# Kernel optimization log

Measured on AMD Instinct MI355X. Metric: run time of the kernel, lower is better.

Reference implementation:

```python
import jax, jax.numpy as jnp
import numpy as np

N_NODES = 50000
N_EDGES = 800000
IN_DIM = 58
HID = 100


def _agnn_prop(x, src, dst, beta, num_nodes):
    """PyG AGNNConv: cosine-similarity attention, softmax over in-edges, scatter-add."""
    # F.normalize(x, p=2, dim=-1) with eps clamp
    norm = jnp.sqrt(jnp.sum(x * x, axis=-1, keepdims=True))
    xn = x / jnp.maximum(norm, 1e-12)
    # per-edge attention logit: beta * cos(x_i, x_j)  (i=dst, j=src)
    alpha = beta * jnp.sum(xn[src] * xn[dst], axis=-1)  # [E]
    # numerically stable softmax grouped by destination node
    m = jax.ops.segment_max(alpha, dst, num_segments=num_nodes)  # [N]
    e = jnp.exp(alpha - m[dst])
    den = jax.ops.segment_sum(e, dst, num_segments=num_nodes)  # [N]
    w = e / (den[dst] + 1e-16)  # [E]
    # attention-weighted aggregation of source features
    return jax.ops.segment_sum(x[src] * w[:, None], dst, num_segments=num_nodes)


def setup_inputs() -> dict:
    key = jax.random.key(0)
    ks = jax.random.split(key, 6)
    x = jax.random.normal(ks[0], (N_NODES, IN_DIM), dtype=jnp.float32)
    edge_index = jax.random.randint(ks[1], (2, N_EDGES), 0, N_NODES, dtype=jnp.int64)
    lin1_w = jax.random.normal(ks[2], (HID, IN_DIM), dtype=jnp.float32) * (1.0 / np.sqrt(IN_DIM))
    lin1_b = jax.random.normal(ks[3], (HID,), dtype=jnp.float32) * 0.01
    beta2 = jnp.ones((1,), dtype=jnp.float32)
    lin2_w = jax.random.normal(ks[4], (1, HID), dtype=jnp.float32) * (1.0 / np.sqrt(HID))
    lin2_b = jax.random.normal(ks[5], (1,), dtype=jnp.float32) * 0.01
    return {"x": x, "edge_index": edge_index, "lin1_w": lin1_w, "lin1_b": lin1_b,
            "beta2": beta2, "lin2_w": lin2_w, "lin2_b": lin2_b}


def reference(x, edge_index, lin1_w, lin1_b, beta2, lin2_w, lin2_b):
    num_nodes = x.shape[0]
    # eval mode: dropout is identity
    h = jax.nn.relu(x @ lin1_w.T + lin1_b)  # [N, 100]
    # AGNNConv adds self-loops by default
    loops = jnp.arange(num_nodes, dtype=edge_index.dtype)
    src = jnp.concatenate([edge_index[0], loops])
    dst = jnp.concatenate([edge_index[1], loops])
    h = _agnn_prop(h, src, dst, jnp.float32(1.0), num_nodes)  # prop1: beta fixed at 1
    h = _agnn_prop(h, src, dst, beta2[0], num_nodes)          # prop2: learnable beta
    return h @ lin2_w.T + lin2_b  # [N, 1]
```

## Files before the change

### kernel.cpp

```cpp
#include <hip/hip_runtime.h>
#include <hip/hip_fp16.h>

#define N_NODES 50000
#define E_BASE  800000
#define IN_DIM  58
#define HID     100
#define HP2     128
#define SCAN_BLOCKS ((N_NODES + 255) / 256)

__global__ __launch_bounds__(256) void lin1_kernel(
    const float* __restrict__ x, const float* __restrict__ w,
    const float* __restrict__ b, __half* __restrict__ h,
    float* __restrict__ invn) {
  __shared__ alignas(16) float xs[64 * IN_DIM];
  __shared__ alignas(16) float wsm[IN_DIM * HP2];
  __shared__ float bl[HP2];
  int tid = threadIdx.x;
  int nb = blockIdx.x * 64;
  for (int i = tid; i < 64 * IN_DIM; i += 256) {
    int g = nb * IN_DIM + i;
    xs[i] = (g < N_NODES * IN_DIM) ? x[g] : 0.f;
  }
  for (int i = tid; i < IN_DIM * HP2; i += 256) {
    int k = i / HP2, j = i - k * HP2;
    wsm[i] = (j < HID) ? w[j * IN_DIM + k] : 0.f;
  }
  if (tid < HP2) bl[tid] = (tid < HID) ? b[tid] : 0.f;
  __syncthreads();
  int t_j = tid & 15, t_n = tid >> 4;
  float acc[4][8];
#pragma unroll
  for (int ni = 0; ni < 4; ++ni)
#pragma unroll
    for (int j = 0; j < 8; ++j) acc[ni][j] = bl[8 * t_j + j];
  for (int k = 0; k < IN_DIM; ++k) {
    float xv[4];
#pragma unroll
    for (int ni = 0; ni < 4; ++ni) xv[ni] = xs[(4 * t_n + ni) * IN_DIM + k];
    float4 wa = *(const float4*)&wsm[k * HP2 + 8 * t_j];
    float4 wb = *(const float4*)&wsm[k * HP2 + 8 * t_j + 4];
    float wv[8] = {wa.x, wa.y, wa.z, wa.w, wb.x, wb.y, wb.z, wb.w};
#pragma unroll
    for (int ni = 0; ni < 4; ++ni)
#pragma unroll
      for (int j = 0; j < 8; ++j) acc[ni][j] = fmaf(xv[ni], wv[j], acc[ni][j]);
  }
#pragma unroll
  for (int ni = 0; ni < 4; ++ni) {
    int n = nb + 4 * t_n + ni;
    uint4 st;
    ushort* sp = (ushort*)&st;
    float ss = 0.f;
#pragma unroll
    for (int j = 0; j < 8; ++j) {
      float v = fmaxf(acc[ni][j], 0.f);
      __half hv = __float2half_rn(v);
      sp[j] = __half_as_ushort(hv);
      float vq = __half2float(hv);
      ss = fmaf(vq, vq, ss);
    }
#pragma unroll
    for (int off = 1; off < 16; off <<= 1) ss += __shfl_xor(ss, off);
    if (n < N_NODES) {
      *((uint4*)(h + (size_t)n * HP2) + t_j) = st;
      if (t_j == 0) invn[n] = 1.f / fmaxf(sqrtf(ss), 1e-12f);
    }
  }
}

__global__ __launch_bounds__(256) void hist_kernel(
    const int* __restrict__ ei, int* __restrict__ deg) {
  int i = blockIdx.x * 256 + threadIdx.x;
  if (i >= E_BASE / 4) return;
  int4 d4 = ((const int4*)(ei + E_BASE))[i];
  atomicAdd(&deg[d4.x], 1);
  atomicAdd(&deg[d4.y], 1);
  atomicAdd(&deg[d4.z], 1);
  atomicAdd(&deg[d4.w], 1);
}

__global__ __launch_bounds__(256) void scan_blocks_kernel(
    const int* __restrict__ deg, int* __restrict__ blocksum) {
  __shared__ int sh[4];
  int idx = blockIdx.x * 256 + threadIdx.x;
  int v = (idx < N_NODES) ? deg[idx] + 1 : 0;
#pragma unroll
  for (int off = 32; off; off >>= 1) v += __shfl_xor(v, off);
  if ((threadIdx.x & 63) == 0) sh[threadIdx.x >> 6] = v;
  __syncthreads();
  if (threadIdx.x == 0) blocksum[blockIdx.x] = sh[0] + sh[1] + sh[2] + sh[3];
}

__global__ __launch_bounds__(256) void scan_top_kernel(int* __restrict__ blocksum) {
  __shared__ int sh[256];
  int t = threadIdx.x;
  sh[t] = (t < SCAN_BLOCKS) ? blocksum[t] : 0;
  __syncthreads();
  for (int off = 1; off < 256; off <<= 1) {
    int v = (t >= off) ? sh[t - off] : 0;
    __syncthreads();
    sh[t] += v;
    __syncthreads();
  }
  if (t < SCAN_BLOCKS) blocksum[t] = (t == 0) ? 0 : sh[t - 1];
}

__global__ __launch_bounds__(256) void scan_apply_kernel(
    const int* __restrict__ deg, const int* __restrict__ blockoff,
    int* __restrict__ rowstart, int* __restrict__ cur,
    int* __restrict__ src_csr) {
  __shared__ int sh[256];
  int t = threadIdx.x;
  int idx = blockIdx.x * 256 + t;
  int v = (idx < N_NODES) ? deg[idx] + 1 : 0;
  sh[t] = v;
  __syncthreads();
  for (int off = 1; off < 256; off <<= 1) {
    int u = (t >= off) ? sh[t - off] : 0;
    __syncthreads();
    sh[t] += u;
    __syncthreads();
  }
  int excl = blockoff[blockIdx.x] + sh[t] - v;
  if (idx < N_NODES) {
    rowstart[idx] = excl;
    src_csr[excl] = idx;
    cur[idx] = excl + 1;
  }
  if (idx == N_NODES - 1) rowstart[N_NODES] = excl + v;
}

__global__ __launch_bounds__(256) void scatter_kernel(
    const int* __restrict__ ei, int* __restrict__ cur,
    int* __restrict__ src_csr) {
  int i = blockIdx.x * 256 + threadIdx.x;
  if (i >= E_BASE / 4) return;
  int4 s4 = ((const int4*)ei)[i];
  int4 d4 = ((const int4*)(ei + E_BASE))[i];
  int p;
  p = atomicAdd(&cur[d4.x], 1); src_csr[p] = s4.x;
  p = atomicAdd(&cur[d4.y], 1); src_csr[p] = s4.y;
  p = atomicAdd(&cur[d4.z], 1); src_csr[p] = s4.z;
  p = atomicAdd(&cur[d4.w], 1); src_csr[p] = s4.w;
}

template<bool WRITE_INVN, bool FINAL>
__global__ __launch_bounds__(256) void prop_kernel(
    const __half* __restrict__ h, const float* __restrict__ invn,
    const int* __restrict__ src_csr, const int* __restrict__ rowstart,
    const float* __restrict__ beta_ptr,
    __half* __restrict__ out_feat, float* __restrict__ out_invn,
    const float* __restrict__ w2, const float* __restrict__ b2,
    float* __restrict__ out_scalar) {
  int node = (blockIdx.x * 256 + threadIdx.x) >> 6;
  int lane = threadIdx.x & 63;
  if (node >= N_NODES) return;
  int lq = lane & 15, q = lane >> 4;
  float beta = beta_ptr ? beta_ptr[0] : 1.0f;
  float B = fabsf(beta);
  int start = rowstart[node], end = rowstart[node + 1];
  int deg = end - start;
  float ind = invn[node];
  uint4 dv = *((const uint4*)(h + (size_t)node * HP2) + lq);
  const __half* dh = (const __half*)&dv;
  float d[8];
#pragma unroll
  for (int j = 0; j < 8; ++j) d[j] = __half2float(dh[j]) * ind;
  float s = 0.f;
  float acc[8];
#pragma unroll
  for (int j = 0; j < 8; ++j) acc[j] = 0.f;
  int nt = (deg + 3) >> 2;
  for (int r = 0; r < nt; ++r) {
    int e = 4 * r + q;
    bool valid = e < deg;
    int p = start + (valid ? e : 0);
    int sn = src_csr[p];
    float iv = invn[sn];
    uint4 vv = *((const uint4*)(h + (size_t)sn * HP2) + lq);
    const __half* vh = (const __half*)&vv;
    float vf[8];
#pragma unroll
    for (int j = 0; j < 8; ++j) vf[j] = __half2float(vh[j]);
    float t = 0.f;
#pragma unroll
    for (int j = 0; j < 8; ++j) t = fmaf(vf[j], d[j], t);
#pragma unroll
    for (int off = 8; off; off >>= 1) t += __shfl_xor(t, off);
    float a = valid ? beta * t * iv : -1e30f;
    float wgt = __expf(a - B);
    s += wgt;
#pragma unroll
    for (int j = 0; j < 8; ++j) acc[j] = fmaf(wgt, vf[j], acc[j]);
  }
#pragma unroll
  for (int off = 16; off <= 32; off <<= 1) {
    s += __shfl_xor(s, off);
#pragma unroll
    for (int j = 0; j < 8; ++j) acc[j] += __shfl_xor(acc[j], off);
  }
  float invden = 1.f / (s + 1e-16f);
  if (!FINAL) {
    uint4 st;
    ushort* sp = (ushort*)&st;
    float ss = 0.f;
#pragma unroll
    for (int j = 0; j < 8; ++j) {
      __half hv = __float2half_rn(acc[j] * invden);
      sp[j] = __half_as_ushort(hv);
      float vq = __half2float(hv);
      ss = fmaf(vq, vq, ss);
    }
    if (q == 0) *((uint4*)(out_feat + (size_t)node * HP2) + lq) = st;
    if (WRITE_INVN) {
#pragma unroll
      for (int off = 1; off < 16; off <<= 1) ss += __shfl_xor(ss, off);
      if (lane == 0) out_invn[node] = 1.f / fmaxf(sqrtf(ss), 1e-12f);
    }
  } else {
    float qq = 0.f;
#pragma unroll
    for (int j = 0; j < 8; ++j) {
      int f = 8 * lq + j;
      float wv = (f < HID) ? w2[f] : 0.f;
      qq = fmaf(acc[j] * invden, wv, qq);
    }
#pragma unroll
    for (int off = 8; off; off >>= 1) qq += __shfl_xor(qq, off);
    if (lane == 0) out_scalar[node] = qq + b2[0];
  }
}

extern "C" void kernel_launch(void* const* d_in, const int* in_sizes, int n_in,
                              void* d_out, int out_size, void* d_ws, size_t ws_size,
                              hipStream_t stream) {
  const float* x      = (const float*)d_in[0];
  const int*   ei     = (const int*)d_in[1];
  const float* lin1_w = (const float*)d_in[2];
  const float* lin1_b = (const float*)d_in[3];
  const float* beta2  = (const float*)d_in[4];
  const float* lin2_w = (const float*)d_in[5];
  const float* lin2_b = (const float*)d_in[6];
  float* out = (float*)d_out;

  char* wsb = (char*)d_ws;
  __half* h1 = (__half*)wsb;                       wsb += (size_t)N_NODES * HP2 * 2;
  __half* h2 = (__half*)wsb;                       wsb += (size_t)N_NODES * HP2 * 2;
  float* invn1 = (float*)wsb;                      wsb += N_NODES * 4;
  float* invn2 = (float*)wsb;                      wsb += N_NODES * 4;
  int* deg      = (int*)wsb;                       wsb += N_NODES * 4;
  int* rowstart = (int*)wsb;                       wsb += (N_NODES + 1) * 4;
  int* cur      = (int*)wsb;                       wsb += N_NODES * 4;
  int* src_csr  = (int*)wsb;                       wsb += (size_t)(E_BASE + N_NODES) * 4;
  int* blocksum = (int*)wsb;                       wsb += SCAN_BLOCKS * 4;

  lin1_kernel<<<(N_NODES + 63) / 64, 256, 0, stream>>>(x, lin1_w, lin1_b, h1, invn1);

  hipMemsetAsync(deg, 0, N_NODES * sizeof(int), stream);
  hist_kernel<<<(E_BASE / 4 + 255) / 256, 256, 0, stream>>>(ei, deg);
  scan_blocks_kernel<<<SCAN_BLOCKS, 256, 0, stream>>>(deg, blocksum);
  scan_top_kernel<<<1, 256, 0, stream>>>(blocksum);
  scan_apply_kernel<<<SCAN_BLOCKS, 256, 0, stream>>>(deg, blocksum, rowstart, cur, src_csr);
  scatter_kernel<<<(E_BASE / 4 + 255) / 256, 256, 0, stream>>>(ei, cur, src_csr);

  prop_kernel<true, false><<<(N_NODES + 3) / 4, 256, 0, stream>>>(
      h1, invn1, src_csr, rowstart, nullptr, h2, invn2, nullptr, nullptr, nullptr);

  prop_kernel<false, true><<<(N_NODES + 3) / 4, 256, 0, stream>>>(
      h2, invn2, src_csr, rowstart, beta2, nullptr, nullptr, lin2_w, lin2_b, out);
}
```

Baseline: 300.7 us.

## Fold top-level scan into apply kernel and widen prop edge parallelism with prefetch

Removes the single-block scan_top kernel: each scan_apply block now redundantly scans all block sums in shared memory alongside its local scan, saving one launch. The prop kernel now has 8 lanes per edge, each handling 16 features, so 8 edges are processed per iteration instead of 4. It also software-prefetches the next edge's index, norm and feature row before computing the current one, to hide gather latency. This raises register use (16-wide acc/d arrays plus prefetch copies), which may reduce occupancy.

```diff
diff --git a/kernel.cpp b/kernel.cpp
--- a/kernel.cpp
+++ b/kernel.cpp
@@ -91,37 +91,28 @@
   if (threadIdx.x == 0) blocksum[blockIdx.x] = sh[0] + sh[1] + sh[2] + sh[3];
 }
 
-__global__ __launch_bounds__(256) void scan_top_kernel(int* __restrict__ blocksum) {
-  __shared__ int sh[256];
-  int t = threadIdx.x;
-  sh[t] = (t < SCAN_BLOCKS) ? blocksum[t] : 0;
-  __syncthreads();
-  for (int off = 1; off < 256; off <<= 1) {
-    int v = (t >= off) ? sh[t - off] : 0;
-    __syncthreads();
-    sh[t] += v;
-    __syncthreads();
-  }
-  if (t < SCAN_BLOCKS) blocksum[t] = (t == 0) ? 0 : sh[t - 1];
-}
-
 __global__ __launch_bounds__(256) void scan_apply_kernel(
-    const int* __restrict__ deg, const int* __restrict__ blockoff,
+    const int* __restrict__ deg, const int* __restrict__ blocksum,
     int* __restrict__ rowstart, int* __restrict__ cur,
     int* __restrict__ src_csr) {
+  __shared__ int top[256];
   __shared__ int sh[256];
   int t = threadIdx.x;
   int idx = blockIdx.x * 256 + t;
+  top[t] = (t < SCAN_BLOCKS) ? blocksum[t] : 0;
   int v = (idx < N_NODES) ? deg[idx] + 1 : 0;
   sh[t] = v;
   __syncthreads();
   for (int off = 1; off < 256; off <<= 1) {
-    int u = (t >= off) ? sh[t - off] : 0;
+    int a = (t >= off) ? top[t - off] : 0;
+    int b = (t >= off) ? sh[t - off] : 0;
     __syncthreads();
-    sh[t] += u;
+    top[t] += a;
+    sh[t] += b;
     __syncthreads();
   }
-  int excl = blockoff[blockIdx.x] + sh[t] - v;
+  int blockoff = (blockIdx.x == 0) ? 0 : top[blockIdx.x - 1];
+  int excl = blockoff + sh[t] - v;
   if (idx < N_NODES) {
     rowstart[idx] = excl;
     src_csr[excl] = idx;
@@ -155,78 +146,118 @@
   int node = (blockIdx.x * 256 + threadIdx.x) >> 6;
   int lane = threadIdx.x & 63;
   if (node >= N_NODES) return;
-  int lq = lane & 15, q = lane >> 4;
+  int lq = lane & 7;
+  int q  = lane >> 3;
   float beta = beta_ptr ? beta_ptr[0] : 1.0f;
   float B = fabsf(beta);
   int start = rowstart[node], end = rowstart[node + 1];
   int deg = end - start;
   float ind = invn[node];
-  uint4 dv = *((const uint4*)(h + (size_t)node * HP2) + lq);
-  const __half* dh = (const __half*)&dv;
-  float d[8];
-#pragma unroll
-  for (int j = 0; j < 8; ++j) d[j] = __half2float(dh[j]) * ind;
+  const uint4* drow = (const uint4*)(h + (size_t)node * HP2);
+  uint4 da = drow[2 * lq], db = drow[2 * lq + 1];
+  float d[16];
+  {
+    const __half* ha = (const __half*)&da;
+    const __half* hb = (const __half*)&db;
+#pragma unroll
+    for (int j = 0; j < 8; ++j) {
+      d[j]     = __half2float(ha[j]) * ind;
+      d[8 + j] = __half2float(hb[j]) * ind;
+    }
+  }
   float s = 0.f;
-  float acc[8];
-#pragma unroll
-  for (int j = 0; j < 8; ++j) acc[j] = 0.f;
-  int nt = (deg + 3) >> 2;
+  float acc[16];
+#pragma unroll
+  for (int j = 0; j < 16; ++j) acc[j] = 0.f;
+  int nt = (deg + 7) >> 3;
+  bool valid = q < deg;
+  int p0 = start + (valid ? q : 0);
+  int sn = src_csr[p0];
+  float iv = invn[sn];
+  const uint4* rp = (const uint4*)(h + (size_t)sn * HP2);
+  uint4 va = rp[2 * lq], vb = rp[2 * lq + 1];
   for (int r = 0; r < nt; ++r) {
-    int e = 4 * r + q;
-    bool valid = e < deg;
-    int p = start + (valid ? e : 0);
-    int sn = src_csr[p];
-    float iv = invn[sn];
-    uint4 vv = *((const uint4*)(h + (size_t)sn * HP2) + lq);
-    const __half* vh = (const __half*)&vv;
-    float vf[8];
-#pragma unroll
-    for (int j = 0; j < 8; ++j) vf[j] = __half2float(vh[j]);
+    bool valid2 = false;
+    float iv2 = 0.f;
+    uint4 va2 = va, vb2 = vb;
+    if (r + 1 < nt) {
+      int e2 = 8 * (r + 1) + q;
+      valid2 = e2 < deg;
+      int p2 = start + (valid2 ? e2 : 0);
+      int sn2 = src_csr[p2];
+      iv2 = invn[sn2];
+      const uint4* rp2 = (const uint4*)(h + (size_t)sn2 * HP2);
+      va2 = rp2[2 * lq];
+      vb2 = rp2[2 * lq + 1];
+    }
+    float vf[16];
+    {
+      const __half* ha = (const __half*)&va;
+      const __half* hb = (const __half*)&vb;
+#pragma unroll
+      for (int j = 0; j < 8; ++j) {
+        vf[j]     = __half2float(ha[j]);
+        vf[8 + j] = __half2float(hb[j]);
+      }
+    }
     float t = 0.f;
 #pragma unroll
-    for (int j = 0; j < 8; ++j) t = fmaf(vf[j], d[j], t);
-#pragma unroll
-    for (int off = 8; off; off >>= 1) t += __shfl_xor(t, off);
+    for (int j = 0; j < 16; ++j) t = fmaf(vf[j], d[j], t);
+#pragma unroll
+    for (int off = 1; off <= 4; off <<= 1) t += __shfl_xor(t, off);
     float a = valid ? beta * t * iv : -1e30f;
     float wgt = __expf(a - B);
     s += wgt;
 #pragma unroll
-    for (int j = 0; j < 8; ++j) acc[j] = fmaf(wgt, vf[j], acc[j]);
-  }
-#pragma unroll
-  for (int off = 16; off <= 32; off <<= 1) {
+    for (int j = 0; j < 16; ++j) acc[j] = fmaf(wgt, vf[j], acc[j]);
+    valid = valid2; iv = iv2; va = va2; vb = vb2;
+  }
+#pragma unroll
+  for (int off = 8; off <= 32; off <<= 1) {
     s += __shfl_xor(s, off);
 #pragma unroll
-    for (int j = 0; j < 8; ++j) acc[j] += __shfl_xor(acc[j], off);
+    for (int j = 0; j < 16; ++j) acc[j] += __shfl_xor(acc[j], off);
   }
   float invden = 1.f / (s + 1e-16f);
   if (!FINAL) {
-    uint4 st;
-    ushort* sp = (ushort*)&st;
+    uint4 sta, stb;
+    ushort* pa = (ushort*)&sta;
+    ushort* pb = (ushort*)&stb;
     float ss = 0.f;
 #pragma unroll
     for (int j = 0; j < 8; ++j) {
       __half hv = __float2half_rn(acc[j] * invden);
-      sp[j] = __half_as_ushort(hv);
+      pa[j] = __half_as_ushort(hv);
       float vq = __half2float(hv);
       ss = fmaf(vq, vq, ss);
     }
-    if (q == 0) *((uint4*)(out_feat + (size_t)node * HP2) + lq) = st;
+#pragma unroll
+    for (int j = 0; j < 8; ++j) {
+      __half hv = __float2half_rn(acc[8 + j] * invden);
+      pb[j] = __half_as_ushort(hv);
+      float vq = __half2float(hv);
+      ss = fmaf(vq, vq, ss);
+    }
+    if (q == 0) {
+      uint4* orow = (uint4*)(out_feat + (size_t)node * HP2);
+      orow[2 * lq] = sta;
+      orow[2 * lq + 1] = stb;
+    }
     if (WRITE_INVN) {
 #pragma unroll
-      for (int off = 1; off < 16; off <<= 1) ss += __shfl_xor(ss, off);
+      for (int off = 1; off <= 4; off <<= 1) ss += __shfl_xor(ss, off);
       if (lane == 0) out_invn[node] = 1.f / fmaxf(sqrtf(ss), 1e-12f);
     }
   } else {
     float qq = 0.f;
 #pragma unroll
-    for (int j = 0; j < 8; ++j) {
-      int f = 8 * lq + j;
+    for (int j = 0; j < 16; ++j) {
+      int f = 16 * lq + j;
       float wv = (f < HID) ? w2[f] : 0.f;
       qq = fmaf(acc[j] * invden, wv, qq);
     }
 #pragma unroll
-    for (int off = 8; off; off >>= 1) qq += __shfl_xor(qq, off);
+    for (int off = 1; off <= 4; off <<= 1) qq += __shfl_xor(qq, off);
     if (lane == 0) out_scalar[node] = qq + b2[0];
   }
 }
@@ -259,7 +290,6 @@
   hipMemsetAsync(deg, 0, N_NODES * sizeof(int), stream);
   hist_kernel<<<(E_BASE / 4 + 255) / 256, 256, 0, stream>>>(ei, deg);
   scan_blocks_kernel<<<SCAN_BLOCKS, 256, 0, stream>>>(deg, blocksum);
-  scan_top_kernel<<<1, 256, 0, stream>>>(blocksum);
   scan_apply_kernel<<<SCAN_BLOCKS, 256, 0, stream>>>(deg, blocksum, rowstart, cur, src_csr);
   scatter_kernel<<<(E_BASE / 4 + 255) / 256, 256, 0, stream>>>(ei, cur, src_csr);
 
```

New measurement: 297.7 us. No clear change (-1.0%).

## Fuse CSR build into one cooperative kernel with rank-based scatter

Applied to the files above, without the earlier changes.

Replaces the memset plus five separate CSR-construction kernels with a single cooperative kernel that uses grid-wide syncs between the histogram, block-scan, top-scan, apply and scatter phases. The histogram now records each edge's atomic return value as a rank, so the scatter phase writes to rowstart+1+rank without a second round of atomics on a cursor array. This removes several launch gaps and one set of contended atomics, at the cost of an extra rank buffer (one int per edge) and the overhead of grid.sync on a 1024-block cooperative launch.

```diff
diff --git a/kernel.cpp b/kernel.cpp
--- a/kernel.cpp
+++ b/kernel.cpp
@@ -1,5 +1,8 @@
 #include <hip/hip_runtime.h>
 #include <hip/hip_fp16.h>
+#include <hip/hip_cooperative_groups.h>
+
+namespace cg = cooperative_groups;
 
 #define N_NODES 50000
 #define E_BASE  800000
@@ -7,6 +10,7 @@
 #define HID     100
 #define HP2     128
 #define SCAN_BLOCKS ((N_NODES + 255) / 256)
+#define CSR_GRID 1024
 
 __global__ __launch_bounds__(256) void lin1_kernel(
     const float* __restrict__ x, const float* __restrict__ w,
@@ -68,80 +72,86 @@
   }
 }
 
-__global__ __launch_bounds__(256) void hist_kernel(
-    const int* __restrict__ ei, int* __restrict__ deg) {
-  int i = blockIdx.x * 256 + threadIdx.x;
-  if (i >= E_BASE / 4) return;
-  int4 d4 = ((const int4*)(ei + E_BASE))[i];
-  atomicAdd(&deg[d4.x], 1);
-  atomicAdd(&deg[d4.y], 1);
-  atomicAdd(&deg[d4.z], 1);
-  atomicAdd(&deg[d4.w], 1);
-}
-
-__global__ __launch_bounds__(256) void scan_blocks_kernel(
-    const int* __restrict__ deg, int* __restrict__ blocksum) {
-  __shared__ int sh[4];
-  int idx = blockIdx.x * 256 + threadIdx.x;
-  int v = (idx < N_NODES) ? deg[idx] + 1 : 0;
-#pragma unroll
-  for (int off = 32; off; off >>= 1) v += __shfl_xor(v, off);
-  if ((threadIdx.x & 63) == 0) sh[threadIdx.x >> 6] = v;
-  __syncthreads();
-  if (threadIdx.x == 0) blocksum[blockIdx.x] = sh[0] + sh[1] + sh[2] + sh[3];
-}
-
-__global__ __launch_bounds__(256) void scan_top_kernel(int* __restrict__ blocksum) {
+__global__ __launch_bounds__(256) void build_csr_kernel(
+    const int* __restrict__ ei, int* __restrict__ deg, int* __restrict__ rank,
+    int* __restrict__ blocksum, int* __restrict__ rowstart,
+    int* __restrict__ src_csr) {
+  cg::grid_group grid = cg::this_grid();
   __shared__ int sh[256];
-  int t = threadIdx.x;
-  sh[t] = (t < SCAN_BLOCKS) ? blocksum[t] : 0;
-  __syncthreads();
-  for (int off = 1; off < 256; off <<= 1) {
-    int v = (t >= off) ? sh[t - off] : 0;
+  __shared__ int top[256];
+  int tid = threadIdx.x;
+  int gtid = blockIdx.x * 256 + tid;
+  const int nthreads = CSR_GRID * 256;
+
+  for (int i = gtid; i < N_NODES; i += nthreads) deg[i] = 0;
+  grid.sync();
+
+  for (int i = gtid; i < E_BASE / 4; i += nthreads) {
+    int4 d4 = ((const int4*)(ei + E_BASE))[i];
+    int r0 = atomicAdd(&deg[d4.x], 1);
+    int r1 = atomicAdd(&deg[d4.y], 1);
+    int r2 = atomicAdd(&deg[d4.z], 1);
+    int r3 = atomicAdd(&deg[d4.w], 1);
+    ((int4*)rank)[i] = make_int4(r0, r1, r2, r3);
+  }
+  grid.sync();
+
+  if (blockIdx.x < SCAN_BLOCKS) {
+    int idx = blockIdx.x * 256 + tid;
+    int v = (idx < N_NODES) ? deg[idx] + 1 : 0;
+#pragma unroll
+    for (int off = 32; off; off >>= 1) v += __shfl_xor(v, off);
+    if (tid == 0) sh[0] = v;
+    if (tid == 64) sh[1] = v;
+    if (tid == 128) sh[2] = v;
+    if (tid == 192) sh[3] = v;
     __syncthreads();
-    sh[t] += v;
+    if (tid == 0) blocksum[blockIdx.x] = sh[0] + sh[1] + sh[2] + sh[3];
+  }
+  grid.sync();
+
+  if (blockIdx.x == 0) {
+    top[tid] = (tid < SCAN_BLOCKS) ? blocksum[tid] : 0;
     __syncthreads();
-  }
-  if (t < SCAN_BLOCKS) blocksum[t] = (t == 0) ? 0 : sh[t - 1];
-}
-
-__global__ __launch_bounds__(256) void scan_apply_kernel(
-    const int* __restrict__ deg, const int* __restrict__ blockoff,
-    int* __restrict__ rowstart, int* __restrict__ cur,
-    int* __restrict__ src_csr) {
-  __shared__ int sh[256];
-  int t = threadIdx.x;
-  int idx = blockIdx.x * 256 + t;
-  int v = (idx < N_NODES) ? deg[idx] + 1 : 0;
-  sh[t] = v;
-  __syncthreads();
-  for (int off = 1; off < 256; off <<= 1) {
-    int u = (t >= off) ? sh[t - off] : 0;
+    for (int off = 1; off < 256; off <<= 1) {
+      int v = (tid >= off) ? top[tid - off] : 0;
+      __syncthreads();
+      top[tid] += v;
+      __syncthreads();
+    }
+    if (tid < SCAN_BLOCKS) blocksum[tid] = (tid == 0) ? 0 : top[tid - 1];
+  }
+  grid.sync();
+
+  if (blockIdx.x < SCAN_BLOCKS) {
+    int idx = blockIdx.x * 256 + tid;
+    int v = (idx < N_NODES) ? deg[idx] + 1 : 0;
+    sh[tid] = v;
     __syncthreads();
-    sh[t] += u;
-    __syncthreads();
-  }
-  int excl = blockoff[blockIdx.x] + sh[t] - v;
-  if (idx < N_NODES) {
-    rowstart[idx] = excl;
-    src_csr[excl] = idx;
-    cur[idx] = excl + 1;
-  }
-  if (idx == N_NODES - 1) rowstart[N_NODES] = excl + v;
-}
-
-__global__ __launch_bounds__(256) void scatter_kernel(
-    const int* __restrict__ ei, int* __restrict__ cur,
-    int* __restrict__ src_csr) {
-  int i = blockIdx.x * 256 + threadIdx.x;
-  if (i >= E_BASE / 4) return;
-  int4 s4 = ((const int4*)ei)[i];
-  int4 d4 = ((const int4*)(ei + E_BASE))[i];
-  int p;
-  p = atomicAdd(&cur[d4.x], 1); src_csr[p] = s4.x;
-  p = atomicAdd(&cur[d4.y], 1); src_csr[p] = s4.y;
-  p = atomicAdd(&cur[d4.z], 1); src_csr[p] = s4.z;
-  p = atomicAdd(&cur[d4.w], 1); src_csr[p] = s4.w;
+    for (int off = 1; off < 256; off <<= 1) {
+      int u = (tid >= off) ? sh[tid - off] : 0;
+      __syncthreads();
+      sh[tid] += u;
+      __syncthreads();
+    }
+    int excl = blocksum[blockIdx.x] + sh[tid] - v;
+    if (idx < N_NODES) {
+      rowstart[idx] = excl;
+      src_csr[excl] = idx;
+    }
+    if (idx == N_NODES - 1) rowstart[N_NODES] = excl + v;
+  }
+  grid.sync();
+
+  for (int i = gtid; i < E_BASE / 4; i += nthreads) {
+    int4 s4 = ((const int4*)ei)[i];
+    int4 d4 = ((const int4*)(ei + E_BASE))[i];
+    int4 r4 = ((const int4*)rank)[i];
+    src_csr[rowstart[d4.x] + 1 + r4.x] = s4.x;
+    src_csr[rowstart[d4.y] + 1 + r4.y] = s4.y;
+    src_csr[rowstart[d4.z] + 1 + r4.z] = s4.z;
+    src_csr[rowstart[d4.w] + 1 + r4.w] = s4.w;
+  }
 }
 
 template<bool WRITE_INVN, bool FINAL>
@@ -249,19 +259,22 @@
   float* invn1 = (float*)wsb;                      wsb += N_NODES * 4;
   float* invn2 = (float*)wsb;                      wsb += N_NODES * 4;
   int* deg      = (int*)wsb;                       wsb += N_NODES * 4;
+  int* rank     = (int*)wsb;                       wsb += (size_t)E_BASE * 4;
+  int* blocksum = (int*)wsb;                       wsb += 256 * 4;
   int* rowstart = (int*)wsb;                       wsb += (N_NODES + 1) * 4;
-  int* cur      = (int*)wsb;                       wsb += N_NODES * 4;
   int* src_csr  = (int*)wsb;                       wsb += (size_t)(E_BASE + N_NODES) * 4;
-  int* blocksum = (int*)wsb;                       wsb += SCAN_BLOCKS * 4;
 
   lin1_kernel<<<(N_NODES + 63) / 64, 256, 0, stream>>>(x, lin1_w, lin1_b, h1, invn1);
 
-  hipMemsetAsync(deg, 0, N_NODES * sizeof(int), stream);
-  hist_kernel<<<(E_BASE / 4 + 255) / 256, 256, 0, stream>>>(ei, deg);
-  scan_blocks_kernel<<<SCAN_BLOCKS, 256, 0, stream>>>(deg, blocksum);
-  scan_top_kernel<<<1, 256, 0, stream>>>(blocksum);
-  scan_apply_kernel<<<SCAN_BLOCKS, 256, 0, stream>>>(deg, blocksum, rowstart, cur, src_csr);
-  scatter_kernel<<<(E_BASE / 4 + 255) / 256, 256, 0, stream>>>(ei, cur, src_csr);
+  {
+    const int* ei_a = ei;
+    int* deg_a = deg; int* rank_a = rank; int* bs_a = blocksum;
+    int* rs_a = rowstart; int* sc_a = src_csr;
+    void* args[] = {(void*)&ei_a, (void*)&deg_a, (void*)&rank_a,
+                    (void*)&bs_a, (void*)&rs_a, (void*)&sc_a};
+    hipLaunchCooperativeKernel((void*)build_csr_kernel, dim3(CSR_GRID),
+                               dim3(256), args, 0, stream);
+  }
 
   prop_kernel<true, false><<<(N_NODES + 3) / 4, 256, 0, stream>>>(
       h1, invn1, src_csr, rowstart, nullptr, h2, invn2, nullptr, nullptr, nullptr);
```

Result: slower. 739.2 us (+145.8%).

## Build CSR with atomic ranks, fold memset and top scan into other kernels

Applied to the files above, without the earlier changes.

Histogram atomics now return each edge's rank within its destination row, which is stored and reused by the scatter pass instead of a second round of atomics on a cursor array. Zeroing of the degree array moves into the lin1 kernel, replacing a separate memset. The single-block top-level scan is folded into scan_apply, with each block recomputing the block-offset prefix. This removes two launches and one atomic pass, but adds a rank buffer write and read plus a rowstart gather in scatter.

```diff
diff --git a/kernel.cpp b/kernel.cpp
--- a/kernel.cpp
+++ b/kernel.cpp
@@ -11,12 +11,14 @@
 __global__ __launch_bounds__(256) void lin1_kernel(
     const float* __restrict__ x, const float* __restrict__ w,
     const float* __restrict__ b, __half* __restrict__ h,
-    float* __restrict__ invn) {
+    float* __restrict__ invn, int* __restrict__ deg) {
   __shared__ alignas(16) float xs[64 * IN_DIM];
   __shared__ alignas(16) float wsm[IN_DIM * HP2];
   __shared__ float bl[HP2];
   int tid = threadIdx.x;
   int nb = blockIdx.x * 64;
+  int gtid = blockIdx.x * 256 + tid;
+  if (gtid < N_NODES) deg[gtid] = 0;
   for (int i = tid; i < 64 * IN_DIM; i += 256) {
     int g = nb * IN_DIM + i;
     xs[i] = (g < N_NODES * IN_DIM) ? x[g] : 0.f;
@@ -69,14 +71,15 @@
 }
 
 __global__ __launch_bounds__(256) void hist_kernel(
-    const int* __restrict__ ei, int* __restrict__ deg) {
+    const int* __restrict__ ei, int* __restrict__ deg, int* __restrict__ rank) {
   int i = blockIdx.x * 256 + threadIdx.x;
   if (i >= E_BASE / 4) return;
   int4 d4 = ((const int4*)(ei + E_BASE))[i];
-  atomicAdd(&deg[d4.x], 1);
-  atomicAdd(&deg[d4.y], 1);
-  atomicAdd(&deg[d4.z], 1);
-  atomicAdd(&deg[d4.w], 1);
+  int r0 = atomicAdd(&deg[d4.x], 1);
+  int r1 = atomicAdd(&deg[d4.y], 1);
+  int r2 = atomicAdd(&deg[d4.z], 1);
+  int r3 = atomicAdd(&deg[d4.w], 1);
+  ((int4*)rank)[i] = make_int4(r0, r1, r2, r3);
 }
 
 __global__ __launch_bounds__(256) void scan_blocks_kernel(
@@ -91,57 +94,46 @@
   if (threadIdx.x == 0) blocksum[blockIdx.x] = sh[0] + sh[1] + sh[2] + sh[3];
 }
 
-__global__ __launch_bounds__(256) void scan_top_kernel(int* __restrict__ blocksum) {
-  __shared__ int sh[256];
-  int t = threadIdx.x;
-  sh[t] = (t < SCAN_BLOCKS) ? blocksum[t] : 0;
-  __syncthreads();
-  for (int off = 1; off < 256; off <<= 1) {
-    int v = (t >= off) ? sh[t - off] : 0;
-    __syncthreads();
-    sh[t] += v;
-    __syncthreads();
-  }
-  if (t < SCAN_BLOCKS) blocksum[t] = (t == 0) ? 0 : sh[t - 1];
-}
-
 __global__ __launch_bounds__(256) void scan_apply_kernel(
-    const int* __restrict__ deg, const int* __restrict__ blockoff,
-    int* __restrict__ rowstart, int* __restrict__ cur,
-    int* __restrict__ src_csr) {
+    const int* __restrict__ deg, const int* __restrict__ blocksum,
+    int* __restrict__ rowstart, int* __restrict__ src_csr) {
+  __shared__ int top[256];
   __shared__ int sh[256];
   int t = threadIdx.x;
   int idx = blockIdx.x * 256 + t;
+  top[t] = (t < SCAN_BLOCKS) ? blocksum[t] : 0;
   int v = (idx < N_NODES) ? deg[idx] + 1 : 0;
   sh[t] = v;
   __syncthreads();
   for (int off = 1; off < 256; off <<= 1) {
-    int u = (t >= off) ? sh[t - off] : 0;
+    int a = (t >= off) ? top[t - off] : 0;
+    int b = (t >= off) ? sh[t - off] : 0;
     __syncthreads();
-    sh[t] += u;
+    top[t] += a;
+    sh[t] += b;
     __syncthreads();
   }
-  int excl = blockoff[blockIdx.x] + sh[t] - v;
+  int blockoff = (blockIdx.x == 0) ? 0 : top[blockIdx.x - 1];
+  int excl = blockoff + sh[t] - v;
   if (idx < N_NODES) {
     rowstart[idx] = excl;
     src_csr[excl] = idx;
-    cur[idx] = excl + 1;
   }
   if (idx == N_NODES - 1) rowstart[N_NODES] = excl + v;
 }
 
 __global__ __launch_bounds__(256) void scatter_kernel(
-    const int* __restrict__ ei, int* __restrict__ cur,
-    int* __restrict__ src_csr) {
+    const int* __restrict__ ei, const int* __restrict__ rowstart,
+    const int* __restrict__ rank, int* __restrict__ src_csr) {
   int i = blockIdx.x * 256 + threadIdx.x;
   if (i >= E_BASE / 4) return;
   int4 s4 = ((const int4*)ei)[i];
   int4 d4 = ((const int4*)(ei + E_BASE))[i];
-  int p;
-  p = atomicAdd(&cur[d4.x], 1); src_csr[p] = s4.x;
-  p = atomicAdd(&cur[d4.y], 1); src_csr[p] = s4.y;
-  p = atomicAdd(&cur[d4.z], 1); src_csr[p] = s4.z;
-  p = atomicAdd(&cur[d4.w], 1); src_csr[p] = s4.w;
+  int4 r4 = ((const int4*)rank)[i];
+  src_csr[rowstart[d4.x] + 1 + r4.x] = s4.x;
+  src_csr[rowstart[d4.y] + 1 + r4.y] = s4.y;
+  src_csr[rowstart[d4.z] + 1 + r4.z] = s4.z;
+  src_csr[rowstart[d4.w] + 1 + r4.w] = s4.w;
 }
 
 template<bool WRITE_INVN, bool FINAL>
@@ -249,19 +241,17 @@
   float* invn1 = (float*)wsb;                      wsb += N_NODES * 4;
   float* invn2 = (float*)wsb;                      wsb += N_NODES * 4;
   int* deg      = (int*)wsb;                       wsb += N_NODES * 4;
+  int* rank     = (int*)wsb;                       wsb += (size_t)E_BASE * 4;
+  int* blocksum = (int*)wsb;                       wsb += 256 * 4;
   int* rowstart = (int*)wsb;                       wsb += (N_NODES + 1) * 4;
-  int* cur      = (int*)wsb;                       wsb += N_NODES * 4;
   int* src_csr  = (int*)wsb;                       wsb += (size_t)(E_BASE + N_NODES) * 4;
-  int* blocksum = (int*)wsb;                       wsb += SCAN_BLOCKS * 4;
-
-  lin1_kernel<<<(N_NODES + 63) / 64, 256, 0, stream>>>(x, lin1_w, lin1_b, h1, invn1);
-
-  hipMemsetAsync(deg, 0, N_NODES * sizeof(int), stream);
-  hist_kernel<<<(E_BASE / 4 + 255) / 256, 256, 0, stream>>>(ei, deg);
+
+  lin1_kernel<<<(N_NODES + 63) / 64, 256, 0, stream>>>(x, lin1_w, lin1_b, h1, invn1, deg);
+
+  hist_kernel<<<(E_BASE / 4 + 255) / 256, 256, 0, stream>>>(ei, deg, rank);
   scan_blocks_kernel<<<SCAN_BLOCKS, 256, 0, stream>>>(deg, blocksum);
-  scan_top_kernel<<<1, 256, 0, stream>>>(blocksum);
-  scan_apply_kernel<<<SCAN_BLOCKS, 256, 0, stream>>>(deg, blocksum, rowstart, cur, src_csr);
-  scatter_kernel<<<(E_BASE / 4 + 255) / 256, 256, 0, stream>>>(ei, cur, src_csr);
+  scan_apply_kernel<<<SCAN_BLOCKS, 256, 0, stream>>>(deg, blocksum, rowstart, src_csr);
+  scatter_kernel<<<(E_BASE / 4 + 255) / 256, 256, 0, stream>>>(ei, rowstart, rank, src_csr);
 
   prop_kernel<true, false><<<(N_NODES + 3) / 4, 256, 0, stream>>>(
       h1, invn1, src_csr, rowstart, nullptr, h2, invn2, nullptr, nullptr, nullptr);
```

Result: faster. 263.6 us (-12.3%).
